# Optimization experiments

Measured on AMD Instinct MI355X. Metric: run time of the kernel, lower is better.

Reference implementation:

```python
import jax, jax.numpy as jnp
import numpy as np

B, L, D = 4, 1024, 256
LN_EPS = 1e-5


def _layernorm(x, g, b):
    mu = jnp.mean(x, axis=-1, keepdims=True)
    var = jnp.mean((x - mu) ** 2, axis=-1, keepdims=True)
    return (x - mu) * jax.lax.rsqrt(var + LN_EPS) * g + b


def setup_inputs() -> dict:
    key = jax.random.key(0)
    ks = jax.random.split(key, 8)
    s = 1.0 / np.sqrt(D)  # torch Linear default init bound
    x = jax.random.normal(ks[0], (B, L, D), jnp.float32)
    Wq = jax.random.uniform(ks[1], (D, D), jnp.float32, -s, s)
    Wk = jax.random.uniform(ks[2], (D, D), jnp.float32, -s, s)
    Wv = jax.random.uniform(ks[3], (D, D), jnp.float32, -s, s)
    beta_w = jnp.zeros((1, D), jnp.float32)          # init.constant_(weight, 0.0)
    beta_b = jnp.full((1,), -4.0, jnp.float32)       # init.constant_(bias, -4.0)
    decay = jnp.full((1,), 0.99, jnp.float32)
    Wo = jax.random.uniform(ks[4], (D, D), jnp.float32, -s, s)
    bo = jax.random.uniform(ks[5], (D,), jnp.float32, -s, s)
    ln_g = jnp.ones((D,), jnp.float32)
    ln_b = jnp.zeros((D,), jnp.float32)
    lnp_g = jnp.ones((D,), jnp.float32)
    lnp_b = jnp.zeros((D,), jnp.float32)
    return {"x": x, "Wq": Wq, "Wk": Wk, "Wv": Wv, "beta_w": beta_w,
            "beta_b": beta_b, "decay": decay, "Wo": Wo, "bo": bo,
            "ln_g": ln_g, "ln_b": ln_b, "lnp_g": lnp_g, "lnp_b": lnp_b}


def reference(x, Wq, Wk, Wv, beta_w, beta_b, decay, Wo, bo, ln_g, ln_b, lnp_g, lnp_b):
    # projections over all tokens (big GEMMs)
    q = x @ Wq.T                                    # [B,L,D]
    k = x @ Wk.T
    v = x @ Wv.T
    phi_q = _layernorm(jax.nn.elu(q) + 1.0, lnp_g, lnp_b)
    phi_k = _layernorm(jax.nn.elu(k) + 1.0, lnp_g, lnp_b)
    beta = jax.nn.sigmoid(x @ beta_w.T + beta_b)    # [B,L,1]
    df = jax.nn.sigmoid(decay)[0]                   # scalar decay factor

    # time-major inputs for the sequential fast-weight recurrence
    pq_t = jnp.swapaxes(phi_q, 0, 1)                # [L,B,D]
    pk_t = jnpp = jnp.swapaxes(phi_k, 0, 1)
    v_t = jnp.swapaxes(v, 0, 1)
    b_t = jnp.swapaxes(beta, 0, 1)                  # [L,B,1]

    def step(W, inp):
        pq, pk, vt, bt = inp                        # [B,D],[B,D],[B,D],[B,1]
        retrieved = jnp.einsum('bij,bj->bi', W, pq)
        v_bar = jnp.einsum('bij,bj->bi', W, pk)
        # W <- decay*W + (beta*(v - v_bar)) outer phi_k
        W = df * W + (bt * (vt - v_bar))[:, :, None] * pk[:, None, :]
        return W, retrieved

    W0 = jnp.zeros((B, D, D), x.dtype)
    _, ys = jax.lax.scan(step, W0, (pq_t, pk_t, v_t, b_t))  # ys: [L,B,D]
    y = jnp.swapaxes(ys, 0, 1)                      # [B,L,D]
    y = _layernorm(y, ln_g, ln_b)
    return y @ Wo.T + bo
```

## Files before the change

kernel.cpp:

```cpp
#include <hip/hip_runtime.h>
#include <math.h>

#define BB 4
#define LL 1024
#define DD 256
#define NT (BB*LL)
#define LN_EPS 1e-5f

#define SEG 128
#define WARM 32

#define OFF_BAND 0
#define OFF_PQ   (8*NT)
#define OFF_PK   (OFF_PQ + NT*DD)
#define OFF_V    (OFF_PK + NT*DD)
#define OFF_Y    (OFF_V + NT*DD)
#define OFF_LNY  (OFF_Y + NT*DD)
#define OFF_BETA (OFF_LNY + NT*DD)

typedef __attribute__((ext_vector_type(8))) short short8;
typedef __attribute__((ext_vector_type(4))) float f32x4;
typedef __attribute__((ext_vector_type(2))) float f32x2;

#define DPP_ADD(x, ctrl) ((x) + __uint_as_float(__builtin_amdgcn_update_dpp( \
        0u, __float_as_uint(x), (ctrl), 0xf, 0xf, true)))
#define DPP_RED6(x) x = DPP_ADD(x, 0x111); x = DPP_ADD(x, 0x112); \
                    x = DPP_ADD(x, 0x114); x = DPP_ADD(x, 0x118); \
                    x = DPP_ADD(x, 0x142); x = DPP_ADD(x, 0x143);

__device__ __forceinline__ float dot4f(float4 a, float4 b) {
    return fmaf(a.x, b.x, a.y * b.y) + fmaf(a.z, b.z, a.w * b.w);
}
__device__ __forceinline__ float rdl63(float x) {
    return __uint_as_float((unsigned)__builtin_amdgcn_readlane(__float_as_uint(x), 63));
}
__device__ __forceinline__ unsigned short f2bf(float f) {
    unsigned u = __float_as_uint(f);
    unsigned r = (u + 0x7fffu + ((u >> 16) & 1u)) >> 16;
    return (unsigned short)r;
}

__device__ __forceinline__ f32x2 pk_mul(f32x2 a, f32x2 b) {
    f32x2 d; asm("v_pk_mul_f32 %0, %1, %2" : "=v"(d) : "v"(a), "v"(b)); return d;
}
__device__ __forceinline__ f32x2 pk_fma(f32x2 a, f32x2 b, f32x2 c) {
    f32x2 d; asm("v_pk_fma_f32 %0, %1, %2, %3" : "=v"(d) : "v"(a), "v"(b), "v"(c)); return d;
}
__device__ __forceinline__ float dot4pk(f32x2 w01, f32x2 w23, float4 b) {
    f32x2 blo = {b.x, b.y}, bhi = {b.z, b.w};
    f32x2 t = pk_mul(w01, blo);
    t = pk_fma(w23, bhi, t);
    return t.x + t.y;
}

__global__ __launch_bounds__(256)
void cast_all_kernel(const float* __restrict__ x, const float* __restrict__ Wq,
                     const float* __restrict__ Wk, const float* __restrict__ Wv,
                     const float* __restrict__ beta_w, const float* __restrict__ beta_b,
                     unsigned short* __restrict__ xb, unsigned short* __restrict__ wb,
                     float* __restrict__ betas)
{
    int b = blockIdx.x;
    if (b < 1024) {
        const int lane = threadIdx.x & 63;
        const int t = b * 4 + (threadIdx.x >> 6);
        size_t idx = (size_t)b * 1024 + (size_t)threadIdx.x * 4;
        float4 v = *(const float4*)(x + idx);
        ushort4 o;
        o.x = f2bf(v.x); o.y = f2bf(v.y); o.z = f2bf(v.z); o.w = f2bf(v.w);
        *(ushort4*)(xb + idx) = o;
        float4 bw4 = *(const float4*)(beta_w + lane * 4);
        float bd = dot4f(v, bw4);
        DPP_RED6(bd)
        if (lane == 63) betas[t] = 1.f / (1.f + expf(-(bd + beta_b[0])));
    } else {
        int wsel = (b - 1024) >> 6;
        const float* src = (wsel == 0) ? Wq : (wsel == 1) ? Wk : Wv;
        unsigned short* dst = wb + (size_t)wsel * 65536;
        size_t idx = (size_t)((b - 1024) & 63) * 1024 + (size_t)threadIdx.x * 4;
        float4 v = *(const float4*)(src + idx);
        ushort4 o;
        o.x = f2bf(v.x); o.y = f2bf(v.y); o.z = f2bf(v.z); o.w = f2bf(v.w);
        *(ushort4*)(dst + idx) = o;
    }
}

__global__ __launch_bounds__(256)
void cast_wo_kernel(const float* __restrict__ Wo, unsigned short* __restrict__ wob)
{
    size_t idx = (size_t)blockIdx.x * 1024 + (size_t)threadIdx.x * 4;
    float4 v = *(const float4*)(Wo + idx);
    ushort4 o;
    o.x = f2bf(v.x); o.y = f2bf(v.y); o.z = f2bf(v.z); o.w = f2bf(v.w);
    *(ushort4*)(wob + idx) = o;
}

__device__ __forceinline__
void gemm_bf16_body(const unsigned short* __restrict__ A,
                    const unsigned short* __restrict__ W,
                    const float* __restrict__ bias, float* __restrict__ C,
                    int tile_m, int tile_n)
{
    const int w = threadIdx.x >> 6;
    const int l = threadIdx.x & 63;
    const int wm = (w >> 1) * 32, wn = (w & 1) * 32;
    const int kb = (l >> 4) * 8;

    const unsigned short* Ap = A + (size_t)(tile_m + wm + (l & 15)) * DD + kb;
    const unsigned short* Wp = W + (size_t)(tile_n + wn + (l & 15)) * DD + kb;

    f32x4 acc00 = {0.f,0.f,0.f,0.f}, acc01 = {0.f,0.f,0.f,0.f};
    f32x4 acc10 = {0.f,0.f,0.f,0.f}, acc11 = {0.f,0.f,0.f,0.f};

    #pragma unroll
    for (int ks = 0; ks < DD; ks += 32) {
        short8 a0 = *(const short8*)(Ap + ks);
        short8 a1 = *(const short8*)(Ap + 16*DD + ks);
        short8 b0 = *(const short8*)(Wp + ks);
        short8 b1 = *(const short8*)(Wp + 16*DD + ks);
        acc00 = __builtin_amdgcn_mfma_f32_16x16x32_bf16(a0, b0, acc00, 0, 0, 0);
        acc01 = __builtin_amdgcn_mfma_f32_16x16x32_bf16(a0, b1, acc01, 0, 0, 0);
        acc10 = __builtin_amdgcn_mfma_f32_16x16x32_bf16(a1, b0, acc10, 0, 0, 0);
        acc11 = __builtin_amdgcn_mfma_f32_16x16x32_bf16(a1, b1, acc11, 0, 0, 0);
    }

    const int r0 = (l >> 4) * 4;
    const int c0 = l & 15;
    #pragma unroll
    for (int i = 0; i < 2; ++i) {
        #pragma unroll
        for (int j = 0; j < 2; ++j) {
            const f32x4 a = (i==0) ? (j==0?acc00:acc01) : (j==0?acc10:acc11);
            int row = tile_m + wm + i*16 + r0;
            int col = tile_n + wn + j*16 + c0;
            float bv = bias ? bias[col] : 0.f;
            #pragma unroll
            for (int r = 0; r < 4; ++r)
                C[(size_t)(row + r) * DD + col] = a[r] + bv;
        }
    }
}

__global__ __launch_bounds__(256)
void gemm_qkv_bf16_kernel(const unsigned short* __restrict__ xb,
                          const unsigned short* __restrict__ wb,
                          float* __restrict__ q, float* __restrict__ k,
                          float* __restrict__ v)
{
    const unsigned short* W = wb + (size_t)blockIdx.z * 65536;
    float* C = (blockIdx.z == 0) ? q : (blockIdx.z == 1) ? k : v;
    gemm_bf16_body(xb, W, nullptr, C, blockIdx.x * 64, blockIdx.y * 64);
}

__global__ __launch_bounds__(256)
void gemm_out_bf16_kernel(const unsigned short* __restrict__ lnyb,
                          const unsigned short* __restrict__ wob,
                          const float* __restrict__ bo, float* __restrict__ C)
{
    gemm_bf16_body(lnyb, wob, bo, C, blockIdx.x * 64, blockIdx.y * 64);
}

__global__ __launch_bounds__(256)
void phi_kernel(const float* __restrict__ q, const float* __restrict__ k,
                float* __restrict__ v, const float* __restrict__ betas,
                const float* __restrict__ lnp_g, const float* __restrict__ lnp_b,
                float* __restrict__ pq, float* __restrict__ pk)
{
    const int t = blockIdx.x * 4 + (threadIdx.x >> 6);
    const int lane = threadIdx.x & 63;
    const int col = lane * 4;
    const size_t base = (size_t)t * DD + col;

    float4 q4 = *(const float4*)(q + base);
    float4 k4 = *(const float4*)(k + base);

    float4 eq, ek;
    eq.x = q4.x > 0.f ? q4.x + 1.f : expf(q4.x);
    eq.y = q4.y > 0.f ? q4.y + 1.f : expf(q4.y);
    eq.z = q4.z > 0.f ? q4.z + 1.f : expf(q4.z);
    eq.w = q4.w > 0.f ? q4.w + 1.f : expf(q4.w);
    ek.x = k4.x > 0.f ? k4.x + 1.f : expf(k4.x);
    ek.y = k4.y > 0.f ? k4.y + 1.f : expf(k4.y);
    ek.z = k4.z > 0.f ? k4.z + 1.f : expf(k4.z);
    ek.w = k4.w > 0.f ? k4.w + 1.f : expf(k4.w);

    float s0 = eq.x + eq.y + eq.z + eq.w;
    float s1 = dot4f(eq, eq);
    float s2 = ek.x + ek.y + ek.z + ek.w;
    float s3 = dot4f(ek, ek);

    DPP_RED6(s0) DPP_RED6(s1) DPP_RED6(s2) DPP_RED6(s3)
    float T0 = rdl63(s0), T1 = rdl63(s1), T2 = rdl63(s2), T3 = rdl63(s3);

    float mu_q = T0 * (1.f/DD);
    float rs_q = rsqrtf(T1 * (1.f/DD) - mu_q*mu_q + LN_EPS);
    float mu_k = T2 * (1.f/DD);
    float rs_k = rsqrtf(T3 * (1.f/DD) - mu_k*mu_k + LN_EPS);
    float beta = betas[t];

    float4 g4 = *(const float4*)(lnp_g + col);
    float4 b4 = *(const float4*)(lnp_b + col);
    float4 oq, ok;
    oq.x = (eq.x - mu_q) * rs_q * g4.x + b4.x;
    oq.y = (eq.y - mu_q) * rs_q * g4.y + b4.y;
    oq.z = (eq.z - mu_q) * rs_q * g4.z + b4.z;
    oq.w = (eq.w - mu_q) * rs_q * g4.w + b4.w;
    ok.x = (ek.x - mu_k) * rs_k * g4.x + b4.x;
    ok.y = (ek.y - mu_k) * rs_k * g4.y + b4.y;
    ok.z = (ek.z - mu_k) * rs_k * g4.z + b4.z;
    ok.w = (ek.w - mu_k) * rs_k * g4.w + b4.w;
    *(float4*)(pq + base) = oq;
    *(float4*)(pk + base) = ok;

    float4 v4 = *(const float4*)(v + base);
    v4.x *= beta; v4.y *= beta; v4.z *= beta; v4.w *= beta;
    *(float4*)(v + base) = v4;
}

__global__ __launch_bounds__(256)
void band_kernel(const float* __restrict__ pq, const float* __restrict__ pk,
                 const float* __restrict__ betas, float* __restrict__ band)
{
    const int wv = threadIdx.x >> 6, lane = threadIdx.x & 63;
    const int g = blockIdx.x * 4 + wv;
    const int tt = g & (LL - 1);
    const int col = lane * 4;

    float4 kv = *(const float4*)(pk + (size_t)g * DD + col);
    float4 qv = *(const float4*)(pq + (size_t)g * DD + col);

    float gg1 = 0.f, hh1 = 0.f;
    if (tt >= 1) { float4 km = *(const float4*)(pk + (size_t)(g-1) * DD + col);
                   gg1 = dot4f(km, kv); hh1 = dot4f(km, qv); }

    DPP_RED6(gg1) DPP_RED6(hh1)

    if (lane == 63) {
        float4 a = make_float4(gg1, hh1, betas[g], 0.f);
        *(float4*)(band + (size_t)g * 4) = a;
    }
}

#define RED_ROUND4(mod, pre)                                                    \
    asm(pre                                                                     \
        "v_add_f32 %0, %0, %0 " mod " bound_ctrl:0\n\t"                         \
        "v_add_f32 %1, %1, %1 " mod " bound_ctrl:0\n\t"                         \
        "v_add_f32 %2, %2, %2 " mod " bound_ctrl:0\n\t"                         \
        "v_add_f32 %3, %3, %3 " mod " bound_ctrl:0"                             \
        : "+v"(s0), "+v"(s1), "+v"(p0), "+v"(p1));

#define RED_ROUND2(mod)                                                         \
    asm("s_nop 1\n\t"                                                           \
        "v_add_f32 %0, %0, %0 " mod " bound_ctrl:0\n\t"                         \
        "v_add_f32 %1, %1, %1 " mod " bound_ctrl:0"                             \
        : "+v"(s0), "+v"(s1));

#define STEP2L(ST)                                                              \
  {                                                                             \
    const float* LB = &ldsb[cur][0][0];                                         \
    float4 kk0 = *(const float4*)(LB + 512 + col4);                             \
    float4 kk1 = *(const float4*)(LB + 768 + col4);                             \
    float4 qq0 = *(const float4*)(LB +       col4);                             \
    float4 qq1 = *(const float4*)(LB + 256 + col4);                             \
    float4 sreg = *(const float4*)(gsrc + gof); gof += 2048u;                   \
    float s0 = dot4pk(w01, w23, kk0),      p0 = dot4pk(w01, w23, qq0);          \
    float s1 = dot4pk(w01, w23, kk1) * df, p1 = dot4pk(w01, w23, qq1) * df;     \
    RED_ROUND4("row_shr:1",   "s_nop 1\n\t")                                    \
    RED_ROUND4("row_shr:2",   "")                                               \
    RED_ROUND4("row_shr:4",   "")                                               \
    RED_ROUND4("row_shr:8",   "")                                               \
    RED_ROUND4("row_bcast:15","")                                               \
    RED_ROUND4("row_bcast:31","")                                               \
    asm volatile("s_nop 1");                                                    \
             \
    const float u0v = fmaf(-bA[0].z, s0, vA[0]);                                \
    const float rr0 = p0;                                                       \
    const float vr1 = fmaf(bA[1].x, u0v, s1);                                   \
    const float rr1 = fmaf(bA[1].y, u0v, p1);                                   \
    const float u1v = fmaf(-bA[1].z, vr1, vA[1]);                               \
    bA[0] = *(const float4*)(bdc + bof);                                        \
    bA[1] = *(const float4*)(bdc + bof + 16);                                   \
    vA[0] = *(const float*)(vbc + vof);                                         \
    vA[1] = *(const float*)(vbc + vof + 1024);                                  \
    bof += 32u; vof += 2048u;                                                   \
    const float u0 = rdl63(u0v), u1 = rdl63(u1v);                               \
    const float ud0 = df * u0;                                                  \
    float4 acc;                                                                 \
    acc.x = ud0*kk0.x; acc.y = ud0*kk0.y; acc.z = ud0*kk0.z; acc.w = ud0*kk0.w; \
    acc.x = fmaf(u1, kk1.x, acc.x); acc.y = fmaf(u1, kk1.y, acc.y);             \
    acc.z = fmaf(u1, kk1.z, acc.z); acc.w = fmaf(u1, kk1.w, acc.w);             \
    { f32x2 a01 = {acc.x, acc.y}, a23 = {acc.z, acc.w};                         \
      w01 = pk_fma(df2p, w01, a01); w23 = pk_fma(df2p, w23, a23); }             \
    if (ST) {                                                                   \
        if (lane == 63) {                                                       \
            *(float*)(ybc + yof)        = rr0;                                  \
            *(float*)(ybc + yof + 1024) = rr1;                                  \
        }                                                                       \
    }                                                                           \
    yof += 2048u;                                                               \
    *(float4*)(&ldsb[cur ^ 1][0][0] + (sid << 8) + col4) = sreg;                \
    __syncthreads();                                                            \
    cur ^= 1;                                                                   \
    __builtin_amdgcn_sched_barrier(0);                                          \
  }

#define STEP2LW()                                                               \
  {                                                                             \
    const float* LB = &ldsb[cur][0][0];                                         \
    float4 kk0 = *(const float4*)(LB + 512 + col4);                             \
    float4 kk1 = *(const float4*)(LB + 768 + col4);                             \
    float4 sreg = *(const float4*)(gsrc + gof); gof += 2048u;                   \
    float s0 = dot4pk(w01, w23, kk0);                                           \
    float s1 = dot4pk(w01, w23, kk1) * df;                                      \
    RED_ROUND2("row_shr:1")                                                     \
    RED_ROUND2("row_shr:2")                                                     \
    RED_ROUND2("row_shr:4")                                                     \
    RED_ROUND2("row_shr:8")                                                     \
    RED_ROUND2("row_bcast:15")                                                  \
    RED_ROUND2("row_bcast:31")                                                  \
    asm volatile("s_nop 1");                                                    \
    const float u0v = fmaf(-bA[0].z, s0, vA[0]);                                \
    const float vr1 = fmaf(bA[1].x, u0v, s1);                                   \
    const float u1v = fmaf(-bA[1].z, vr1, vA[1]);                               \
    bA[0] = *(const float4*)(bdc + bof);                                        \
    bA[1] = *(const float4*)(bdc + bof + 16);                                   \
    vA[0] = *(const float*)(vbc + vof);                                         \
    vA[1] = *(const float*)(vbc + vof + 1024);                                  \
    bof += 32u; vof += 2048u;                                                   \
    const float u0 = rdl63(u0v), u1 = rdl63(u1v);                               \
    const float ud0 = df * u0;                                                  \
    float4 acc;                                                                 \
    acc.x = ud0*kk0.x; acc.y = ud0*kk0.y; acc.z = ud0*kk0.z; acc.w = ud0*kk0.w; \
    acc.x = fmaf(u1, kk1.x, acc.x); acc.y = fmaf(u1, kk1.y, acc.y);             \
    acc.z = fmaf(u1, kk1.z, acc.z); acc.w = fmaf(u1, kk1.w, acc.w);             \
    { f32x2 a01 = {acc.x, acc.y}, a23 = {acc.z, acc.w};                         \
      w01 = pk_fma(df2p, w01, a01); w23 = pk_fma(df2p, w23, a23); }             \
    *(float4*)(&ldsb[cur ^ 1][0][0] + (sid << 8) + col4) = sreg;                \
    __syncthreads();                                                            \
    cur ^= 1;                                                                   \
    __builtin_amdgcn_sched_barrier(0);                                          \
  }

__global__ __launch_bounds__(256, 8)
void recur_kernel(const float* __restrict__ pq, const float* __restrict__ pk,
                  const float* __restrict__ vbeta, const float* __restrict__ band,
                  const float* __restrict__ decay, float* __restrict__ y)
{
    const int sl   = blockIdx.x & 31;
    const int rg   = blockIdx.x >> 5;
    const int s    = sl >> 2;
    const int b    = sl & 3;
    const int lane = threadIdx.x & 63;
    const int sid  = threadIdx.x >> 6;
    const int i    = rg * 4 + sid;

    const float df  = 1.f / (1.f + expf(-decay[0]));
    const float df2 = df * df;
    const f32x2 df2p = {df2, df2};

    const float* pqb = pq    + (size_t)b * LL * DD;
    const float* pkb = pk    + (size_t)b * LL * DD;
    const float* vbb = vbeta + (size_t)b * LL * DD;
    const float* bdb = band  + (size_t)b * LL * 4;
    float* yb = y + (size_t)b * LL * DD;
    const char* pqc = (const char*)pqb;
    const char* pkc = (const char*)pkb;
    const char* vbc = (const char*)vbb;
    const char* bdc = (const char*)bdb;
    char* ybc = (char*)yb;
    const int col4 = lane * 4;

    const int t0    = s * SEG;
    const int start = s ? (t0 - WARM) : 0;
    const int nwarm = s ? (WARM / 2) : 0;

    f32x2 w01 = {0.f, 0.f}, w23 = {0.f, 0.f};

    __shared__ float ldsb[2][4][256];

    float4 bA[2]; float vA[2];
    #pragma unroll
    for (int p = 0; p < 2; ++p) {
        bA[p] = *(const float4*)(bdb + (size_t)(start+p) * 4);
        vA[p] = vbb[(size_t)(start+p) * DD + i];
    }

    const char* gsrc = (sid < 2) ? pqc : pkc;
    unsigned gof = (unsigned)(start + (sid & 1)) * 1024u + (unsigned)lane * 16u;

    {
        float4 s0v = *(const float4*)(gsrc + gof);
        *(float4*)(&ldsb[0][0][0] + (sid << 8) + col4) = s0v;
        gof += 2048u;
        __syncthreads();
    }
    int cur = 0;

    unsigned vof = (unsigned)(start+2) * 1024u + (unsigned)i * 4u;
    unsigned bof = (unsigned)(start+2) * 16u;
    unsigned yof = (unsigned)t0        * 1024u + (unsigned)i * 4u;

    for (int it = 0; it < nwarm; ++it) {
        STEP2LW()
    }
    for (int it = 0; it < SEG/2; ++it) {
        STEP2L(1)
    }
}

__global__ __launch_bounds__(256)
void ln_kernel(const float* __restrict__ y, const float* __restrict__ g,
               const float* __restrict__ b, unsigned short* __restrict__ out)
{
    const int t = blockIdx.x * 4 + (threadIdx.x >> 6);
    const int lane = threadIdx.x & 63;
    const int col = lane * 4;
    const size_t base = (size_t)t * DD + col;

    float4 v4 = *(const float4*)(y + base);
    float s0 = v4.x + v4.y + v4.z + v4.w;
    float s1 = dot4f(v4, v4);
    DPP_RED6(s0) DPP_RED6(s1)
    float T0 = rdl63(s0), T1 = rdl63(s1);
    float mu = T0 * (1.f/DD);
    float rs = rsqrtf(T1 * (1.f/DD) - mu*mu + LN_EPS);

    float4 g4 = *(const float4*)(g + col);
    float4 b4 = *(const float4*)(b + col);
    ushort4 o;
    o.x = f2bf((v4.x - mu) * rs * g4.x + b4.x);
    o.y = f2bf((v4.y - mu) * rs * g4.y + b4.y);
    o.z = f2bf((v4.z - mu) * rs * g4.z + b4.z);
    o.w = f2bf((v4.w - mu) * rs * g4.w + b4.w);
    *(ushort4*)(out + base) = o;
}

extern "C" void kernel_launch(void* const* d_in, const int* in_sizes, int n_in,
                              void* d_out, int out_size, void* d_ws, size_t ws_size,
                              hipStream_t stream)
{
    const float* x      = (const float*)d_in[0];
    const float* Wq     = (const float*)d_in[1];
    const float* Wk     = (const float*)d_in[2];
    const float* Wv     = (const float*)d_in[3];
    const float* beta_w = (const float*)d_in[4];
    const float* beta_b = (const float*)d_in[5];
    const float* decay  = (const float*)d_in[6];
    const float* Wo     = (const float*)d_in[7];
    const float* bo     = (const float*)d_in[8];
    const float* ln_g   = (const float*)d_in[9];
    const float* ln_b   = (const float*)d_in[10];
    const float* lnp_g  = (const float*)d_in[11];
    const float* lnp_b  = (const float*)d_in[12];

    float* ws = (float*)d_ws;
    float* band  = ws + OFF_BAND;
    float* pq    = ws + OFF_PQ;
    float* pk    = ws + OFF_PK;
    float* v_st  = ws + OFF_V;
    float* q_st  = ws + OFF_Y;
    float* k_st  = ws + OFF_LNY;
    float* betas = ws + OFF_BETA;

    unsigned short* xb   = (unsigned short*)(ws + OFF_PQ);
    unsigned short* wb   = (unsigned short*)(ws + OFF_PK);
    unsigned short* lnyb = (unsigned short*)(ws + OFF_LNY);
    unsigned short* wob  = (unsigned short*)(ws + OFF_V);

    cast_all_kernel<<<1024 + 192, 256, 0, stream>>>(x, Wq, Wk, Wv, beta_w, beta_b,
                                                    xb, wb, betas);

    gemm_qkv_bf16_kernel<<<dim3(NT/64, DD/64, 3), 256, 0, stream>>>(
        xb, wb, q_st, k_st, v_st);

    phi_kernel<<<NT/4, 256, 0, stream>>>(q_st, k_st, v_st, betas,
                                         lnp_g, lnp_b, pq, pk);

    band_kernel<<<NT/4, 256, 0, stream>>>(pq, pk, betas, band);

    recur_kernel<<<2048, 256, 0, stream>>>(pq, pk, v_st, band, decay, ws + OFF_Y);

    ln_kernel<<<NT/4, 256, 0, stream>>>(ws + OFF_Y, ln_g, ln_b, lnyb);
    cast_wo_kernel<<<64, 256, 0, stream>>>(Wo, wob);
    gemm_out_bf16_kernel<<<dim3(NT/64, DD/64), 256, 0, stream>>>(
        lnyb, wob, bo, (float*)d_out);
}
```

Baseline: 122.7 us.

## Process four timesteps per recurrence step using precomputed 3-lag key Gram band

The recurrence kernel now advances four timesteps per step instead of two. The band kernel precomputes lag-1..3 dot products between keys and queries, prescaled by powers of the decay, into 16-float records per group of four. Each recurrence step then does a single batched DPP reduction over eight dot products and one rank-4 weight update with decay^4, which halves the number of barriers and reduction chains. In exchange it needs more LDS, more registers and a longer serial scalar chain to solve for the four corrections.

```diff
diff --git a/kernel.cpp b/kernel.cpp
--- a/kernel.cpp
+++ b/kernel.cpp
@@ -219,123 +219,199 @@
 
 __global__ __launch_bounds__(256)
 void band_kernel(const float* __restrict__ pq, const float* __restrict__ pk,
-                 const float* __restrict__ betas, float* __restrict__ band)
+                 const float* __restrict__ betas, const float* __restrict__ decay,
+                 float* __restrict__ band)
 {
     const int wv = threadIdx.x >> 6, lane = threadIdx.x & 63;
     const int g = blockIdx.x * 4 + wv;
     const int tt = g & (LL - 1);
     const int col = lane * 4;
+    const float df = 1.f / (1.f + expf(-decay[0]));
 
     float4 kv = *(const float4*)(pk + (size_t)g * DD + col);
     float4 qv = *(const float4*)(pq + (size_t)g * DD + col);
 
-    float gg1 = 0.f, hh1 = 0.f;
+    float gg1 = 0.f, hh1 = 0.f, gg2 = 0.f, hh2 = 0.f, gg3 = 0.f, hh3 = 0.f;
     if (tt >= 1) { float4 km = *(const float4*)(pk + (size_t)(g-1) * DD + col);
                    gg1 = dot4f(km, kv); hh1 = dot4f(km, qv); }
-
-    DPP_RED6(gg1) DPP_RED6(hh1)
+    if (tt >= 2) { float4 km = *(const float4*)(pk + (size_t)(g-2) * DD + col);
+                   gg2 = dot4f(km, kv); hh2 = dot4f(km, qv); }
+    if (tt >= 3) { float4 km = *(const float4*)(pk + (size_t)(g-3) * DD + col);
+                   gg3 = dot4f(km, kv); hh3 = dot4f(km, qv); }
+
+    DPP_RED6(gg1) DPP_RED6(hh1) DPP_RED6(gg2) DPP_RED6(hh2) DPP_RED6(gg3) DPP_RED6(hh3)
 
     if (lane == 63) {
-        float4 a = make_float4(gg1, hh1, betas[g], 0.f);
-        *(float4*)(band + (size_t)g * 4) = a;
-    }
-}
-
-#define RED_ROUND4(mod, pre)                                                    \
+        float* rec = band + (size_t)(g >> 2) * 16;
+        const int j = g & 3;
+        float G1 = gg1, G2 = df*gg2, G3 = df*df*gg3;
+        float H1 = hh1, H2 = df*hh2, H3 = df*df*hh3;
+        float beta = betas[g];
+        if (j == 0)      { rec[12] = beta; }
+        else if (j == 1) { rec[0] = G1; rec[6] = H1; rec[13] = beta; }
+        else if (j == 2) { rec[1] = G1; rec[2] = G2; rec[7] = H1; rec[8] = H2;
+                           rec[14] = beta; }
+        else             { rec[3] = G1; rec[4] = G2; rec[5] = G3; rec[9] = H1;
+                           rec[10] = H2; rec[11] = H3; rec[15] = beta; }
+    }
+}
+
+#define RED_ROUND8(mod, pre)                                                    \
+    asm(pre                                                                     \
+        "v_add_f32 %0, %0, %0 " mod " bound_ctrl:0\n\t"                         \
+        "v_add_f32 %1, %1, %1 " mod " bound_ctrl:0\n\t"                         \
+        "v_add_f32 %2, %2, %2 " mod " bound_ctrl:0\n\t"                         \
+        "v_add_f32 %3, %3, %3 " mod " bound_ctrl:0\n\t"                         \
+        "v_add_f32 %4, %4, %4 " mod " bound_ctrl:0\n\t"                         \
+        "v_add_f32 %5, %5, %5 " mod " bound_ctrl:0\n\t"                         \
+        "v_add_f32 %6, %6, %6 " mod " bound_ctrl:0\n\t"                         \
+        "v_add_f32 %7, %7, %7 " mod " bound_ctrl:0"                             \
+        : "+v"(s0), "+v"(s1), "+v"(s2), "+v"(s3),                               \
+          "+v"(p0), "+v"(p1), "+v"(p2), "+v"(p3));
+
+#define RED_ROUND4S(mod, pre)                                                   \
     asm(pre                                                                     \
         "v_add_f32 %0, %0, %0 " mod " bound_ctrl:0\n\t"                         \
         "v_add_f32 %1, %1, %1 " mod " bound_ctrl:0\n\t"                         \
         "v_add_f32 %2, %2, %2 " mod " bound_ctrl:0\n\t"                         \
         "v_add_f32 %3, %3, %3 " mod " bound_ctrl:0"                             \
-        : "+v"(s0), "+v"(s1), "+v"(p0), "+v"(p1));
-
-#define RED_ROUND2(mod)                                                         \
-    asm("s_nop 1\n\t"                                                           \
-        "v_add_f32 %0, %0, %0 " mod " bound_ctrl:0\n\t"                         \
-        "v_add_f32 %1, %1, %1 " mod " bound_ctrl:0"                             \
-        : "+v"(s0), "+v"(s1));
-
-#define STEP2L(ST)                                                              \
+        : "+v"(s0), "+v"(s1), "+v"(s2), "+v"(s3));
+
+#define STEP4L(ST)                                                              \
   {                                                                             \
     const float* LB = &ldsb[cur][0][0];                                         \
-    float4 kk0 = *(const float4*)(LB + 512 + col4);                             \
-    float4 kk1 = *(const float4*)(LB + 768 + col4);                             \
-    float4 qq0 = *(const float4*)(LB +       col4);                             \
-    float4 qq1 = *(const float4*)(LB + 256 + col4);                             \
-    float4 sreg = *(const float4*)(gsrc + gof); gof += 2048u;                   \
-    float s0 = dot4pk(w01, w23, kk0),      p0 = dot4pk(w01, w23, qq0);          \
-    float s1 = dot4pk(w01, w23, kk1) * df, p1 = dot4pk(w01, w23, qq1) * df;     \
-    RED_ROUND4("row_shr:1",   "s_nop 1\n\t")                                    \
-    RED_ROUND4("row_shr:2",   "")                                               \
-    RED_ROUND4("row_shr:4",   "")                                               \
-    RED_ROUND4("row_shr:8",   "")                                               \
-    RED_ROUND4("row_bcast:15","")                                               \
-    RED_ROUND4("row_bcast:31","")                                               \
+    float4 qq0 = *(const float4*)(LB +        col4);                            \
+    float4 qq1 = *(const float4*)(LB + 256  + col4);                            \
+    float4 qq2 = *(const float4*)(LB + 512  + col4);                            \
+    float4 qq3 = *(const float4*)(LB + 768  + col4);                            \
+    float4 kk0 = *(const float4*)(LB + 1024 + col4);                            \
+    float4 kk1 = *(const float4*)(LB + 1280 + col4);                            \
+    float4 kk2 = *(const float4*)(LB + 1536 + col4);                            \
+    float4 kk3 = *(const float4*)(LB + 1792 + col4);                            \
+    float s0 = dot4pk(w01, w23, kk0),       p0 = dot4pk(w01, w23, qq0);         \
+    float s1 = dot4pk(w01, w23, kk1) * df,  p1 = dot4pk(w01, w23, qq1) * df;    \
+    float s2 = dot4pk(w01, w23, kk2) * df2, p2 = dot4pk(w01, w23, qq2) * df2;   \
+    float s3 = dot4pk(w01, w23, kk3) * df3, p3 = dot4pk(w01, w23, qq3) * df3;   \
+    float4 fG  = *(const float4*)(bdc + gbof);                                  \
+    float4 fG2 = *(const float4*)(bdc + gbof + 16);                             \
+    float4 fH  = *(const float4*)(bdc + gbof + 32);                             \
+    float4 fB  = *(const float4*)(bdc + gbof + 48);                             \
+    gbof += 64u;                                                                \
+    float vA0 = *(const float*)(vbc + vof);                                     \
+    float vA1 = *(const float*)(vbc + vof + 1024);                              \
+    float vA2 = *(const float*)(vbc + vof + 2048);                              \
+    float vA3 = *(const float*)(vbc + vof + 3072);                              \
+    vof += 4096u;                                                               \
+    float4 sq = *(const float4*)(pqc + gqof);                                   \
+    float4 sk = *(const float4*)(pkc + gkof);                                   \
+    gqof += 4096u; gkof += 4096u;                                               \
+    RED_ROUND8("row_shr:1",   "s_nop 1\n\t")                                    \
+    RED_ROUND8("row_shr:2",   "")                                               \
+    RED_ROUND8("row_shr:4",   "")                                               \
+    RED_ROUND8("row_shr:8",   "")                                               \
+    RED_ROUND8("row_bcast:15","")                                               \
+    RED_ROUND8("row_bcast:31","")                                               \
     asm volatile("s_nop 1");                                                    \
-             \
-    const float u0v = fmaf(-bA[0].z, s0, vA[0]);                                \
+         \
+    const float u0v = fmaf(-fB.x, s0, vA0);                                     \
     const float rr0 = p0;                                                       \
-    const float vr1 = fmaf(bA[1].x, u0v, s1);                                   \
-    const float rr1 = fmaf(bA[1].y, u0v, p1);                                   \
-    const float u1v = fmaf(-bA[1].z, vr1, vA[1]);                               \
-    bA[0] = *(const float4*)(bdc + bof);                                        \
-    bA[1] = *(const float4*)(bdc + bof + 16);                                   \
-    vA[0] = *(const float*)(vbc + vof);                                         \
-    vA[1] = *(const float*)(vbc + vof + 1024);                                  \
-    bof += 32u; vof += 2048u;                                                   \
+    const float vr1 = fmaf(fG.x, u0v, s1);                                      \
+    const float rr1 = fmaf(fG2.z, u0v, p1);                                     \
+    const float u1v = fmaf(-fB.y, vr1, vA1);                                    \
+    const float vr2 = fmaf(fG.y, u1v, fmaf(fG.z, u0v, s2));                     \
+    const float rr2 = fmaf(fG2.w, u1v, fmaf(fH.x, u0v, p2));                    \
+    const float u2v = fmaf(-fB.z, vr2, vA2);                                    \
+    const float vr3 = fmaf(fG.w, u2v, fmaf(fG2.x, u1v, fmaf(fG2.y, u0v, s3)));  \
+    const float rr3 = fmaf(fH.y, u2v, fmaf(fH.z, u1v, fmaf(fH.w, u0v, p3)));    \
+    const float u3v = fmaf(-fB.w, vr3, vA3);                                    \
     const float u0 = rdl63(u0v), u1 = rdl63(u1v);                               \
-    const float ud0 = df * u0;                                                  \
+    const float u2 = rdl63(u2v), u3 = rdl63(u3v);                               \
+                         \
+    float4 ka0 = *(const float4*)(LB + 1024 + col4);                            \
+    float4 ka1 = *(const float4*)(LB + 1280 + col4);                            \
+    float4 ka2 = *(const float4*)(LB + 1536 + col4);                            \
+    float4 ka3 = *(const float4*)(LB + 1792 + col4);                            \
     float4 acc;                                                                 \
-    acc.x = ud0*kk0.x; acc.y = ud0*kk0.y; acc.z = ud0*kk0.z; acc.w = ud0*kk0.w; \
-    acc.x = fmaf(u1, kk1.x, acc.x); acc.y = fmaf(u1, kk1.y, acc.y);             \
-    acc.z = fmaf(u1, kk1.z, acc.z); acc.w = fmaf(u1, kk1.w, acc.w);             \
+    acc.x = u0*ka0.x; acc.y = u0*ka0.y; acc.z = u0*ka0.z; acc.w = u0*ka0.w;     \
+    acc.x = fmaf(df, acc.x, u1*ka1.x); acc.y = fmaf(df, acc.y, u1*ka1.y);       \
+    acc.z = fmaf(df, acc.z, u1*ka1.z); acc.w = fmaf(df, acc.w, u1*ka1.w);       \
+    acc.x = fmaf(df, acc.x, u2*ka2.x); acc.y = fmaf(df, acc.y, u2*ka2.y);       \
+    acc.z = fmaf(df, acc.z, u2*ka2.z); acc.w = fmaf(df, acc.w, u2*ka2.w);       \
+    acc.x = fmaf(df, acc.x, u3*ka3.x); acc.y = fmaf(df, acc.y, u3*ka3.y);       \
+    acc.z = fmaf(df, acc.z, u3*ka3.z); acc.w = fmaf(df, acc.w, u3*ka3.w);       \
     { f32x2 a01 = {acc.x, acc.y}, a23 = {acc.z, acc.w};                         \
-      w01 = pk_fma(df2p, w01, a01); w23 = pk_fma(df2p, w23, a23); }             \
+      w01 = pk_fma(df4p, w01, a01); w23 = pk_fma(df4p, w23, a23); }             \
     if (ST) {                                                                   \
         if (lane == 63) {                                                       \
             *(float*)(ybc + yof)        = rr0;                                  \
             *(float*)(ybc + yof + 1024) = rr1;                                  \
+            *(float*)(ybc + yof + 2048) = rr2;                                  \
+            *(float*)(ybc + yof + 3072) = rr3;                                  \
         }                                                                       \
+        yof += 4096u;                                                           \
     }                                                                           \
-    yof += 2048u;                                                               \
-    *(float4*)(&ldsb[cur ^ 1][0][0] + (sid << 8) + col4) = sreg;                \
+    *(float4*)(&ldsb[cur ^ 1][sid][0]     + col4) = sq;                         \
+    *(float4*)(&ldsb[cur ^ 1][4 + sid][0] + col4) = sk;                         \
     __syncthreads();                                                            \
     cur ^= 1;                                                                   \
     __builtin_amdgcn_sched_barrier(0);                                          \
   }
 
-#define STEP2LW()                                                               \
+#define STEP4LW()                                                               \
   {                                                                             \
     const float* LB = &ldsb[cur][0][0];                                         \
-    float4 kk0 = *(const float4*)(LB + 512 + col4);                             \
-    float4 kk1 = *(const float4*)(LB + 768 + col4);                             \
-    float4 sreg = *(const float4*)(gsrc + gof); gof += 2048u;                   \
+    float4 kk0 = *(const float4*)(LB + 1024 + col4);                            \
+    float4 kk1 = *(const float4*)(LB + 1280 + col4);                            \
+    float4 kk2 = *(const float4*)(LB + 1536 + col4);                            \
+    float4 kk3 = *(const float4*)(LB + 1792 + col4);                            \
     float s0 = dot4pk(w01, w23, kk0);                                           \
     float s1 = dot4pk(w01, w23, kk1) * df;                                      \
-    RED_ROUND2("row_shr:1")                                                     \
-    RED_ROUND2("row_shr:2")                                                     \
-    RED_ROUND2("row_shr:4")                                                     \
-    RED_ROUND2("row_shr:8")                                                     \
-    RED_ROUND2("row_bcast:15")                                                  \
-    RED_ROUND2("row_bcast:31")                                                  \
+    float s2 = dot4pk(w01, w23, kk2) * df2;                                     \
+    float s3 = dot4pk(w01, w23, kk3) * df3;                                     \
+    float4 fG  = *(const float4*)(bdc + gbof);                                  \
+    float4 fG2 = *(const float4*)(bdc + gbof + 16);                             \
+    float4 fB  = *(const float4*)(bdc + gbof + 48);                             \
+    gbof += 64u;                                                                \
+    float vA0 = *(const float*)(vbc + vof);                                     \
+    float vA1 = *(const float*)(vbc + vof + 1024);                              \
+    float vA2 = *(const float*)(vbc + vof + 2048);                              \
+    float vA3 = *(const float*)(vbc + vof + 3072);                              \
+    vof += 4096u;                                                               \
+    float4 sq = *(const float4*)(pqc + gqof);                                   \
+    float4 sk = *(const float4*)(pkc + gkof);                                   \
+    gqof += 4096u; gkof += 4096u;                                               \
+    RED_ROUND4S("row_shr:1",   "s_nop 1\n\t")                                   \
+    RED_ROUND4S("row_shr:2",   "")                                              \
+    RED_ROUND4S("row_shr:4",   "")                                              \
+    RED_ROUND4S("row_shr:8",   "")                                              \
+    RED_ROUND4S("row_bcast:15","")                                              \
+    RED_ROUND4S("row_bcast:31","")                                              \
     asm volatile("s_nop 1");                                                    \
-    const float u0v = fmaf(-bA[0].z, s0, vA[0]);                                \
-    const float vr1 = fmaf(bA[1].x, u0v, s1);                                   \
-    const float u1v = fmaf(-bA[1].z, vr1, vA[1]);                               \
-    bA[0] = *(const float4*)(bdc + bof);                                        \
-    bA[1] = *(const float4*)(bdc + bof + 16);                                   \
-    vA[0] = *(const float*)(vbc + vof);                                         \
-    vA[1] = *(const float*)(vbc + vof + 1024);                                  \
-    bof += 32u; vof += 2048u;                                                   \
+    const float u0v = fmaf(-fB.x, s0, vA0);                                     \
+    const float vr1 = fmaf(fG.x, u0v, s1);                                      \
+    const float u1v = fmaf(-fB.y, vr1, vA1);                                    \
+    const float vr2 = fmaf(fG.y, u1v, fmaf(fG.z, u0v, s2));                     \
+    const float u2v = fmaf(-fB.z, vr2, vA2);                                    \
+    const float vr3 = fmaf(fG.w, u2v, fmaf(fG2.x, u1v, fmaf(fG2.y, u0v, s3)));  \
+    const float u3v = fmaf(-fB.w, vr3, vA3);                                    \
     const float u0 = rdl63(u0v), u1 = rdl63(u1v);                               \
-    const float ud0 = df * u0;                                                  \
+    const float u2 = rdl63(u2v), u3 = rdl63(u3v);                               \
+    float4 ka0 = *(const float4*)(LB + 1024 + col4);                            \
+    float4 ka1 = *(const float4*)(LB + 1280 + col4);                            \
+    float4 ka2 = *(const float4*)(LB + 1536 + col4);                            \
+    float4 ka3 = *(const float4*)(LB + 1792 + col4);                            \
     float4 acc;                                                                 \
-    acc.x = ud0*kk0.x; acc.y = ud0*kk0.y; acc.z = ud0*kk0.z; acc.w = ud0*kk0.w; \
-    acc.x = fmaf(u1, kk1.x, acc.x); acc.y = fmaf(u1, kk1.y, acc.y);             \
-    acc.z = fmaf(u1, kk1.z, acc.z); acc.w = fmaf(u1, kk1.w, acc.w);             \
+    acc.x = u0*ka0.x; acc.y = u0*ka0.y; acc.z = u0*ka0.z; acc.w = u0*ka0.w;     \
+    acc.x = fmaf(df, acc.x, u1*ka1.x); acc.y = fmaf(df, acc.y, u1*ka1.y);       \
+    acc.z = fmaf(df, acc.z, u1*ka1.z); acc.w = fmaf(df, acc.w, u1*ka1.w);       \
+    acc.x = fmaf(df, acc.x, u2*ka2.x); acc.y = fmaf(df, acc.y, u2*ka2.y);       \
+    acc.z = fmaf(df, acc.z, u2*ka2.z); acc.w = fmaf(df, acc.w, u2*ka2.w);       \
+    acc.x = fmaf(df, acc.x, u3*ka3.x); acc.y = fmaf(df, acc.y, u3*ka3.y);       \
+    acc.z = fmaf(df, acc.z, u3*ka3.z); acc.w = fmaf(df, acc.w, u3*ka3.w);       \
     { f32x2 a01 = {acc.x, acc.y}, a23 = {acc.z, acc.w};                         \
-      w01 = pk_fma(df2p, w01, a01); w23 = pk_fma(df2p, w23, a23); }             \
-    *(float4*)(&ldsb[cur ^ 1][0][0] + (sid << 8) + col4) = sreg;                \
+      w01 = pk_fma(df4p, w01, a01); w23 = pk_fma(df4p, w23, a23); }             \
+    *(float4*)(&ldsb[cur ^ 1][sid][0]     + col4) = sq;                         \
+    *(float4*)(&ldsb[cur ^ 1][4 + sid][0] + col4) = sk;                         \
     __syncthreads();                                                            \
     cur ^= 1;                                                                   \
     __builtin_amdgcn_sched_barrier(0);                                          \
@@ -355,8 +431,8 @@
     const int i    = rg * 4 + sid;
 
     const float df  = 1.f / (1.f + expf(-decay[0]));
-    const float df2 = df * df;
-    const f32x2 df2p = {df2, df2};
+    const float df2 = df * df, df3 = df2 * df, df4 = df2 * df2;
+    const f32x2 df4p = {df4, df4};
 
     const float* pqb = pq    + (size_t)b * LL * DD;
     const float* pkb = pk    + (size_t)b * LL * DD;
@@ -372,39 +448,34 @@
 
     const int t0    = s * SEG;
     const int start = s ? (t0 - WARM) : 0;
-    const int nwarm = s ? (WARM / 2) : 0;
+    const int nwarm = s ? (WARM / 4) : 0;
 
     f32x2 w01 = {0.f, 0.f}, w23 = {0.f, 0.f};
 
-    __shared__ float ldsb[2][4][256];
-
-    float4 bA[2]; float vA[2];
-    #pragma unroll
-    for (int p = 0; p < 2; ++p) {
-        bA[p] = *(const float4*)(bdb + (size_t)(start+p) * 4);
-        vA[p] = vbb[(size_t)(start+p) * DD + i];
-    }
-
-    const char* gsrc = (sid < 2) ? pqc : pkc;
-    unsigned gof = (unsigned)(start + (sid & 1)) * 1024u + (unsigned)lane * 16u;
+    __shared__ float ldsb[2][8][256];
+
+    unsigned gqof = (unsigned)(start + sid) * 1024u + (unsigned)lane * 16u;
+    unsigned gkof = gqof;
 
     {
-        float4 s0v = *(const float4*)(gsrc + gof);
-        *(float4*)(&ldsb[0][0][0] + (sid << 8) + col4) = s0v;
-        gof += 2048u;
+        float4 a = *(const float4*)(pqc + gqof);
+        float4 c = *(const float4*)(pkc + gkof);
+        *(float4*)(&ldsb[0][sid][0]     + col4) = a;
+        *(float4*)(&ldsb[0][4 + sid][0] + col4) = c;
+        gqof += 4096u; gkof += 4096u;
         __syncthreads();
     }
     int cur = 0;
 
-    unsigned vof = (unsigned)(start+2) * 1024u + (unsigned)i * 4u;
-    unsigned bof = (unsigned)(start+2) * 16u;
-    unsigned yof = (unsigned)t0        * 1024u + (unsigned)i * 4u;
+    unsigned gbof = (unsigned)(start >> 2) * 64u;
+    unsigned vof  = (unsigned)start * 1024u + (unsigned)i * 4u;
+    unsigned yof  = (unsigned)t0    * 1024u + (unsigned)i * 4u;
 
     for (int it = 0; it < nwarm; ++it) {
-        STEP2LW()
-    }
-    for (int it = 0; it < SEG/2; ++it) {
-        STEP2L(1)
+        STEP4LW()
+    }
+    for (int it = 0; it < SEG/4; ++it) {
+        STEP4L(1)
     }
 }
 
@@ -476,7 +547,7 @@
     phi_kernel<<<NT/4, 256, 0, stream>>>(q_st, k_st, v_st, betas,
                                          lnp_g, lnp_b, pq, pk);
 
-    band_kernel<<<NT/4, 256, 0, stream>>>(pq, pk, betas, band);
+    band_kernel<<<NT/4, 256, 0, stream>>>(pq, pk, betas, decay, band);
 
     recur_kernel<<<2048, 256, 0, stream>>>(pq, pk, v_st, band, decay, ws + OFF_Y);
 
```

Measured after the change: 127.7 us. 1.04x slower.
